# Optimization experiments

Measured on AMD Instinct MI355X. Metric: run time of the kernel, lower is better.

## Reference

```python
import jax, jax.numpy as jnp
import numpy as np

N = 100000
E = 1600000
D_IN = 128
D_OUT = 128
BN_EPS = 1e-5


def setup_inputs() -> dict:
    key = jax.random.key(0)
    k1, k2, k3, k4 = jax.random.split(key, 4)
    x = jax.random.normal(k1, (N, D_IN), dtype=jnp.float32)
    edge_index = jax.random.randint(k2, (2, E), 0, N, dtype=jnp.int64)
    # Linear params (torch: y = x @ W.T + b)
    lim = 1.0 / np.sqrt(D_IN)
    W = jax.random.uniform(k3, (D_OUT, D_IN), minval=-lim, maxval=lim, dtype=jnp.float32)
    b = jax.random.uniform(k4, (D_OUT,), minval=-lim, maxval=lim, dtype=jnp.float32)
    # BatchNorm1d affine params (torch defaults: weight=1, bias=0)
    gamma = jnp.ones((D_OUT,), dtype=jnp.float32)
    beta = jnp.zeros((D_OUT,), dtype=jnp.float32)
    return {"x": x, "edge_index": edge_index, "W": W, "b": b,
            "gamma": gamma, "beta": beta, "batch_size": 32}


def reference(x, edge_index, W, b, gamma, beta, batch_size):
    # Linear
    h = x @ W.T + b  # (N, D_OUT)
    num_nodes = h.shape[0]
    row, col = edge_index[0], edge_index[1]
    # Gather neighbor features and scatter-add into destination rows
    agg = jax.ops.segment_sum(h[col], row, num_segments=num_nodes)  # (N, D_OUT)
    cnt = jax.ops.segment_sum(jnp.ones((edge_index.shape[1], 1), dtype=h.dtype),
                              row, num_segments=num_nodes)  # (N, 1)
    agg = agg / (cnt + 1e-8)
    # Residual
    h = h + agg
    # BatchNorm1d, training mode (batch statistics, biased variance)
    mean = jnp.mean(h, axis=0)
    var = jnp.mean((h - mean) ** 2, axis=0)
    out = (h - mean) * jax.lax.rsqrt(var + BN_EPS) * gamma + beta
    return out
```

## Files before the change

### kernel.cpp

```cpp
#include <hip/hip_runtime.h>

#define BN_EPS_F 1e-5f
#define MAXB 128
#define BIN_CHUNK 4096
#define BIN_EPT 16

typedef __attribute__((ext_vector_type(8))) short bf16x8;
typedef __attribute__((ext_vector_type(4))) float f32x4;

static __device__ __forceinline__ float bf2f(unsigned short u) {
  union { unsigned int i; float f; } c; c.i = ((unsigned int)u) << 16; return c.f;
}
static __device__ __forceinline__ unsigned short f2bf(float f) {
  union { float f; unsigned int i; } c; c.f = f;
  unsigned int r = c.i + 0x7FFFu + ((c.i >> 16) & 1u);
  return (unsigned short)(r >> 16);
}

__global__ void wfrag_kernel(const float* __restrict__ W, unsigned short* __restrict__ wfrag) {
  int idx = blockIdx.x * 256 + threadIdx.x;
  int e = idx & 7, l = (idx >> 3) & 63, kk = (idx >> 9) & 3, jt = idx >> 11;
  int j = jt * 16 + (l & 15);
  int k = kk * 32 + ((l >> 4) << 3) + e;
  wfrag[idx] = f2bf(W[j * 128 + k]);
}

__global__ __launch_bounds__(256) void linear_kernel(
    const float* __restrict__ x, const unsigned short* __restrict__ wfrag,
    const float* __restrict__ bias, ushort4* __restrict__ h4, int n) {
  __shared__ unsigned short els[4][16 * 128];
  const int t = threadIdx.x;
  const int w = t >> 6, lane = t & 63;
  const int base = blockIdx.x * 64 + w * 16;
  const int row = base + (lane & 15);
  const int rowc = row < n ? row : (n - 1);
  const float4* xr = reinterpret_cast<const float4*>(x) + (size_t)rowc * 32;
  const bf16x8* bf = reinterpret_cast<const bf16x8*>(wfrag);

  f32x4 acc[8];
#pragma unroll
  for (int jt = 0; jt < 8; ++jt) acc[jt] = (f32x4){0.f, 0.f, 0.f, 0.f};

#pragma unroll
  for (int kk = 0; kk < 4; ++kk) {
    float4 lo = xr[kk * 8 + ((lane >> 4) << 1)];
    float4 hi = xr[kk * 8 + ((lane >> 4) << 1) + 1];
    bf16x8 a;
    a[0] = (short)f2bf(lo.x); a[1] = (short)f2bf(lo.y);
    a[2] = (short)f2bf(lo.z); a[3] = (short)f2bf(lo.w);
    a[4] = (short)f2bf(hi.x); a[5] = (short)f2bf(hi.y);
    a[6] = (short)f2bf(hi.z); a[7] = (short)f2bf(hi.w);
#pragma unroll
    for (int jt = 0; jt < 8; ++jt) {
      bf16x8 b = bf[(jt * 4 + kk) * 64 + lane];
      acc[jt] = __builtin_amdgcn_mfma_f32_16x16x32_bf16(a, b, acc[jt], 0, 0, 0);
    }
  }

  unsigned short* ep = els[w];
#pragma unroll
  for (int jt = 0; jt < 8; ++jt) {
    float bv = bias[jt * 16 + (lane & 15)];
#pragma unroll
    for (int r = 0; r < 4; ++r) {
      int orow = ((lane >> 4) << 2) + r;
      ep[orow * 128 + jt * 16 + (lane & 15)] = f2bf(acc[jt][r] + bv);
    }
  }
  const ushort4* ep4 = reinterpret_cast<const ushort4*>(ep);
#pragma unroll
  for (int i = 0; i < 8; ++i) {
    int idx = i * 64 + lane;
    int r2 = idx >> 5, c4 = idx & 31;
    int grow = base + r2;
    if (grow < n) h4[(size_t)grow * 32 + c4] = ep4[idx];
  }
}

__global__ __launch_bounds__(256) void bucket_hist_kernel(
    const int* __restrict__ row, int* __restrict__ bhist, int e_total, int nb) {
  __shared__ int bh[MAXB];
  const int t = threadIdx.x;
  if (t < MAXB) bh[t] = 0;
  __syncthreads();
  int i = blockIdx.x * 256 + t;
  const int stride = gridDim.x * 256;
  for (; i < e_total; i += stride) atomicAdd(&bh[row[i] >> 10], 1);
  __syncthreads();
  if (t < nb) {
    int c = bh[t];
    if (c) atomicAdd(&bhist[t], c);
  }
}

__global__ void bucket_scan_kernel(const int* __restrict__ bhist, int* __restrict__ bbase,
                                   int* __restrict__ bcursor, int nb, int e_total) {
  __shared__ int sd[MAXB];
  const int t = threadIdx.x;
  int v = (t < nb) ? bhist[t] : 0;
  sd[t] = v;
  __syncthreads();
  for (int off = 1; off < MAXB; off <<= 1) {
    int u = (t >= off) ? sd[t - off] : 0;
    __syncthreads();
    sd[t] += u;
    __syncthreads();
  }
  int excl = sd[t] - v;
  if (t < nb) { bbase[t] = excl; bcursor[t] = excl; }
  if (t == 0) bbase[nb] = e_total;
}

__global__ __launch_bounds__(256) void bin_kernel(
    const int* __restrict__ row, const int* __restrict__ col,
    int* __restrict__ bcursor, unsigned int* __restrict__ pairs, int e_total, int nb) {
  __shared__ int scount[MAXB];
  __shared__ int gbase[MAXB];
  const int t = threadIdx.x;
  if (t < MAXB) scount[t] = 0;
  __syncthreads();
  const int base = blockIdx.x * BIN_CHUNK;
  int bkt[BIN_EPT], slot[BIN_EPT];
  unsigned int pk[BIN_EPT];
#pragma unroll
  for (int k = 0; k < BIN_EPT; ++k) {
    int i = base + t + (k << 8);
    bkt[k] = -1;
    if (i < e_total) {
      int r = row[i], c = col[i];
      bkt[k] = r >> 10;
      pk[k] = ((unsigned int)(r & 1023) << 17) | (unsigned int)c;
      slot[k] = atomicAdd(&scount[bkt[k]], 1);
    }
  }
  __syncthreads();
  if (t < nb) {
    int c = scount[t];
    gbase[t] = c ? atomicAdd(&bcursor[t], c) : 0;
  }
  __syncthreads();
#pragma unroll
  for (int k = 0; k < BIN_EPT; ++k) {
    if (bkt[k] >= 0) pairs[gbase[bkt[k]] + slot[k]] = pk[k];
  }
}

__global__ __launch_bounds__(256) void csr_kernel(
    const unsigned int* __restrict__ pairs, const int* __restrict__ bbase,
    int* __restrict__ rowptr, int* __restrict__ scol, int n, int e_total) {
  __shared__ int lh[1024];
  __shared__ int sscan[256];
  const int b = blockIdx.x;
  const int t = threadIdx.x;
  const int node_base = b << 10;
  const int nn = min(1024, n - node_base);
  const int p0 = bbase[b], p1 = bbase[b + 1];
  for (int j = t; j < 1024; j += 256) lh[j] = 0;
  __syncthreads();
  for (int i = p0 + t; i < p1; i += 256) {
    atomicAdd(&lh[pairs[i] >> 17], 1);
  }
  __syncthreads();
  const int v0 = lh[4 * t + 0], v1 = lh[4 * t + 1], v2 = lh[4 * t + 2], v3 = lh[4 * t + 3];
  const int s = v0 + v1 + v2 + v3;
  sscan[t] = s;
  __syncthreads();
  for (int off = 1; off < 256; off <<= 1) {
    int u = (t >= off) ? sscan[t - off] : 0;
    __syncthreads();
    sscan[t] += u;
    __syncthreads();
  }
  const int excl = sscan[t] - s;
  const int c0 = excl, c1 = excl + v0, c2 = c1 + v1, c3 = c2 + v2;
  if (4 * t + 0 < nn) rowptr[node_base + 4 * t + 0] = p0 + c0;
  if (4 * t + 1 < nn) rowptr[node_base + 4 * t + 1] = p0 + c1;
  if (4 * t + 2 < nn) rowptr[node_base + 4 * t + 2] = p0 + c2;
  if (4 * t + 3 < nn) rowptr[node_base + 4 * t + 3] = p0 + c3;
  __syncthreads();
  lh[4 * t + 0] = c0; lh[4 * t + 1] = c1; lh[4 * t + 2] = c2; lh[4 * t + 3] = c3;
  __syncthreads();
  for (int i = p0 + t; i < p1; i += 256) {
    unsigned int p = pairs[i];
    int pl = atomicAdd(&lh[p >> 17], 1);
    scol[p0 + pl] = (int)(p & 0x1FFFFu);
  }
  if (b == 0 && t == 0) rowptr[n] = e_total;
}

__global__ __launch_bounds__(256) void agg_kernel(
    const ushort4* __restrict__ h4, const int* __restrict__ rowptr,
    const int* __restrict__ scol, float* __restrict__ out,
    float* __restrict__ stat_sum, float* __restrict__ stat_sumsq, int n_nodes) {
  const int t = threadIdx.x;
  const int wave = t >> 6, lane = t & 63;
  const int half = lane >> 5, q = lane & 31;
  float ls0 = 0.f, ls1 = 0.f, ls2 = 0.f, ls3 = 0.f;
  float lq0 = 0.f, lq1 = 0.f, lq2 = 0.f, lq3 = 0.f;
  const int wstride = gridDim.x << 2;
  for (int node = (blockIdx.x << 2) + wave; node < n_nodes; node += wstride) {
    const int r0 = rowptr[node], r1 = rowptr[node + 1];
    float a0 = 0.f, a1 = 0.f, a2 = 0.f, a3 = 0.f;
    int e = r0 + half;
    for (; e + 2 < r1; e += 4) {
      int c0 = scol[e], c1 = scol[e + 2];
      ushort4 v0 = h4[(size_t)c0 * 32 + q];
      ushort4 v1 = h4[(size_t)c1 * 32 + q];
      a0 += bf2f(v0.x) + bf2f(v1.x);
      a1 += bf2f(v0.y) + bf2f(v1.y);
      a2 += bf2f(v0.z) + bf2f(v1.z);
      a3 += bf2f(v0.w) + bf2f(v1.w);
    }
    if (e < r1) {
      int c0 = scol[e];
      ushort4 v0 = h4[(size_t)c0 * 32 + q];
      a0 += bf2f(v0.x); a1 += bf2f(v0.y); a2 += bf2f(v0.z); a3 += bf2f(v0.w);
    }
    a0 += __shfl_xor(a0, 32, 64);
    a1 += __shfl_xor(a1, 32, 64);
    a2 += __shfl_xor(a2, 32, 64);
    a3 += __shfl_xor(a3, 32, 64);
    if (half == 0) {
      ushort4 hv = h4[(size_t)node * 32 + q];
      const float inv = 1.0f / ((float)(r1 - r0) + 1e-8f);
      float v0 = fmaf(a0, inv, bf2f(hv.x));
      float v1 = fmaf(a1, inv, bf2f(hv.y));
      float v2 = fmaf(a2, inv, bf2f(hv.z));
      float v3 = fmaf(a3, inv, bf2f(hv.w));
      float4 o; o.x = v0; o.y = v1; o.z = v2; o.w = v3;
      *reinterpret_cast<float4*>(&out[(size_t)node * 128 + q * 4]) = o;
      ls0 += v0; ls1 += v1; ls2 += v2; ls3 += v3;
      lq0 = fmaf(v0, v0, lq0); lq1 = fmaf(v1, v1, lq1);
      lq2 = fmaf(v2, v2, lq2); lq3 = fmaf(v3, v3, lq3);
    }
  }
  __shared__ float reds[4][128];
  __shared__ float redq[4][128];
  if (half == 0) {
    float4 s; s.x = ls0; s.y = ls1; s.z = ls2; s.w = ls3;
    float4 qq; qq.x = lq0; qq.y = lq1; qq.z = lq2; qq.w = lq3;
    *reinterpret_cast<float4*>(&reds[wave][q * 4]) = s;
    *reinterpret_cast<float4*>(&redq[wave][q * 4]) = qq;
  }
  __syncthreads();
  if (t < 128) {
    float s = reds[0][t] + reds[1][t] + reds[2][t] + reds[3][t];
    float qv = redq[0][t] + redq[1][t] + redq[2][t] + redq[3][t];
    atomicAdd(&stat_sum[t], s);
    atomicAdd(&stat_sumsq[t], qv);
  }
}

__global__ void finalize_kernel(const float* __restrict__ ssum, const float* __restrict__ ssq,
                                const float* __restrict__ gamma, const float* __restrict__ beta,
                                float* __restrict__ scale, float* __restrict__ shift, int n) {
  const int t = threadIdx.x;
  const float invn = 1.0f / (float)n;
  float mean = ssum[t] * invn;
  float var = ssq[t] * invn - mean * mean;
  float sc = gamma[t] * rsqrtf(var + BN_EPS_F);
  scale[t] = sc;
  shift[t] = beta[t] - mean * sc;
}

__global__ __launch_bounds__(256) void bn_kernel(float* __restrict__ out,
                                                 const float* __restrict__ scale,
                                                 const float* __restrict__ shift, int n_nodes) {
  __shared__ float sc[128], sh[128];
  if (threadIdx.x < 128) {
    sc[threadIdx.x] = scale[threadIdx.x];
    sh[threadIdx.x] = shift[threadIdx.x];
  }
  __syncthreads();
  const int total4 = n_nodes * 32;
  int i = blockIdx.x * 256 + threadIdx.x;
  const int stride = gridDim.x * 256;
  float4* o4 = reinterpret_cast<float4*>(out);
  for (; i < total4; i += stride) {
    float4 v = o4[i];
    const int fq = (i & 31) << 2;
    v.x = fmaf(v.x, sc[fq + 0], sh[fq + 0]);
    v.y = fmaf(v.y, sc[fq + 1], sh[fq + 1]);
    v.z = fmaf(v.z, sc[fq + 2], sh[fq + 2]);
    v.w = fmaf(v.w, sc[fq + 3], sh[fq + 3]);
    o4[i] = v;
  }
}

extern "C" void kernel_launch(void* const* d_in, const int* in_sizes, int n_in,
                              void* d_out, int out_size, void* d_ws, size_t ws_size,
                              hipStream_t stream) {
  const float* x     = (const float*)d_in[0];
  const int*   ei    = (const int*)d_in[1];
  const float* W     = (const float*)d_in[2];
  const float* bias  = (const float*)d_in[3];
  const float* gamma = (const float*)d_in[4];
  const float* beta  = (const float*)d_in[5];
  const int n = in_sizes[0] / 128;
  const int e = in_sizes[1] / 2;
  const int* row = ei;
  const int* col = ei + e;
  float* out = (float*)d_out;

  char* base = (char*)d_ws;
  size_t off = 0;
  auto carve = [&](size_t bytes) -> char* {
    char* p = base + off;
    off += (bytes + 255) & ~(size_t)255;
    return p;
  };
  unsigned short* h = (unsigned short*)carve((size_t)n * 128 * 2);
  unsigned short* wfrag = (unsigned short*)carve(128 * 128 * 2);
  unsigned int* pairs = (unsigned int*)carve((size_t)e * 4);
  int*   scol     = (int*)carve((size_t)e * 4);
  int*   rowptr   = (int*)carve((size_t)(n + 1) * 4);
  int*   bcursor  = (int*)carve(MAXB * 4);
  int*   bbase    = (int*)carve((MAXB + 1) * 4);
  float* scale    = (float*)carve(512);
  float* shift    = (float*)carve(512);
  char*  zbase    = base + off;
  int*   bhist    = (int*)carve(MAXB * 4);
  float* ssum     = (float*)carve(512);
  float* ssq      = (float*)carve(512);
  size_t zlen     = (size_t)((base + off) - zbase);
  (void)ws_size; (void)n_in; (void)out_size;

  const int nb = (n + 1023) >> 10;
  const int bin_grid = (e + BIN_CHUNK - 1) / BIN_CHUNK;
  const int lin_grid = (n + 63) / 64;

  hipMemsetAsync(zbase, 0, zlen, stream);
  wfrag_kernel<<<64, 256, 0, stream>>>(W, wfrag);
  linear_kernel<<<lin_grid, 256, 0, stream>>>(x, wfrag, bias, (ushort4*)h, n);
  bucket_hist_kernel<<<256, 256, 0, stream>>>(row, bhist, e, nb);
  bucket_scan_kernel<<<1, MAXB, 0, stream>>>(bhist, bbase, bcursor, nb, e);
  bin_kernel<<<bin_grid, 256, 0, stream>>>(row, col, bcursor, pairs, e, nb);
  csr_kernel<<<nb, 256, 0, stream>>>(pairs, bbase, rowptr, scol, n, e);
  agg_kernel<<<3200, 256, 0, stream>>>((const ushort4*)h, rowptr, scol, out, ssum, ssq, n);
  finalize_kernel<<<1, 128, 0, stream>>>(ssum, ssq, gamma, beta, scale, shift, n);
  bn_kernel<<<2048, 256, 0, stream>>>(out, scale, shift, n);
}
```

Before: 349.0 us.

## Slice h into feature-major column blocks so aggregation gathers fit in cache

The linear output is stored as 8 slices of 16 features (32 bytes per node per slice). The aggregation kernel assigns each block one slice and one node partition, so the gathered working set per slice (about 3.2 MB) can stay in L2/LLC instead of streaming the full 25 MB table randomly. The intermediate aggregated result is stored in bf16 and converted back in the BN kernel, which halves that round trip but adds a rounding step before normalization. CSR buckets also shrink to 512 nodes, doubling the bucket count, and each gather now moves only 4 bytes per lane, which may raise the instruction overhead per edge.

```diff
diff --git a/kernel.cpp b/kernel.cpp
--- a/kernel.cpp
+++ b/kernel.cpp
@@ -1,9 +1,11 @@
 #include <hip/hip_runtime.h>
 
 #define BN_EPS_F 1e-5f
-#define MAXB 128
+#define MAXB 256
+#define BSHIFT 9
 #define BIN_CHUNK 4096
 #define BIN_EPT 16
+#define NPART 400
 
 typedef __attribute__((ext_vector_type(8))) short bf16x8;
 typedef __attribute__((ext_vector_type(4))) float f32x4;
@@ -27,8 +29,8 @@
 
 __global__ __launch_bounds__(256) void linear_kernel(
     const float* __restrict__ x, const unsigned short* __restrict__ wfrag,
-    const float* __restrict__ bias, ushort4* __restrict__ h4, int n) {
-  __shared__ unsigned short els[4][16 * 128];
+    const float* __restrict__ bias, unsigned short* __restrict__ ht, int n) {
+  __shared__ unsigned short els[4][16 * 132];
   const int t = threadIdx.x;
   const int w = t >> 6, lane = t & 63;
   const int base = blockIdx.x * 64 + w * 16;
@@ -64,16 +66,18 @@
 #pragma unroll
     for (int r = 0; r < 4; ++r) {
       int orow = ((lane >> 4) << 2) + r;
-      ep[orow * 128 + jt * 16 + (lane & 15)] = f2bf(acc[jt][r] + bv);
-    }
-  }
-  const ushort4* ep4 = reinterpret_cast<const ushort4*>(ep);
-#pragma unroll
-  for (int i = 0; i < 8; ++i) {
-    int idx = i * 64 + lane;
-    int r2 = idx >> 5, c4 = idx & 31;
-    int grow = base + r2;
-    if (grow < n) h4[(size_t)grow * 32 + c4] = ep4[idx];
+      ep[orow * 132 + jt * 16 + (lane & 15)] = f2bf(acc[jt][r] + bv);
+    }
+  }
+  const int nl = lane >> 2;
+  const int f4 = (lane & 3) << 2;
+  const int gnode = base + nl;
+#pragma unroll
+  for (int jt = 0; jt < 8; ++jt) {
+    if (gnode < n) {
+      ushort4 v = *reinterpret_cast<const ushort4*>(&ep[nl * 132 + jt * 16 + f4]);
+      *reinterpret_cast<ushort4*>(&ht[((size_t)jt * n + gnode) * 16 + f4]) = v;
+    }
   }
 }
 
@@ -81,11 +85,11 @@
     const int* __restrict__ row, int* __restrict__ bhist, int e_total, int nb) {
   __shared__ int bh[MAXB];
   const int t = threadIdx.x;
-  if (t < MAXB) bh[t] = 0;
+  bh[t] = 0;
   __syncthreads();
   int i = blockIdx.x * 256 + t;
   const int stride = gridDim.x * 256;
-  for (; i < e_total; i += stride) atomicAdd(&bh[row[i] >> 10], 1);
+  for (; i < e_total; i += stride) atomicAdd(&bh[row[i] >> BSHIFT], 1);
   __syncthreads();
   if (t < nb) {
     int c = bh[t];
@@ -117,7 +121,7 @@
   __shared__ int scount[MAXB];
   __shared__ int gbase[MAXB];
   const int t = threadIdx.x;
-  if (t < MAXB) scount[t] = 0;
+  scount[t] = 0;
   __syncthreads();
   const int base = blockIdx.x * BIN_CHUNK;
   int bkt[BIN_EPT], slot[BIN_EPT];
@@ -128,8 +132,8 @@
     bkt[k] = -1;
     if (i < e_total) {
       int r = row[i], c = col[i];
-      bkt[k] = r >> 10;
-      pk[k] = ((unsigned int)(r & 1023) << 17) | (unsigned int)c;
+      bkt[k] = r >> BSHIFT;
+      pk[k] = ((unsigned int)(r & ((1 << BSHIFT) - 1)) << 17) | (unsigned int)c;
       slot[k] = atomicAdd(&scount[bkt[k]], 1);
     }
   }
@@ -148,21 +152,21 @@
 __global__ __launch_bounds__(256) void csr_kernel(
     const unsigned int* __restrict__ pairs, const int* __restrict__ bbase,
     int* __restrict__ rowptr, int* __restrict__ scol, int n, int e_total) {
-  __shared__ int lh[1024];
+  __shared__ int lh[1 << BSHIFT];
   __shared__ int sscan[256];
   const int b = blockIdx.x;
   const int t = threadIdx.x;
-  const int node_base = b << 10;
-  const int nn = min(1024, n - node_base);
+  const int node_base = b << BSHIFT;
+  const int nn = min(1 << BSHIFT, n - node_base);
   const int p0 = bbase[b], p1 = bbase[b + 1];
-  for (int j = t; j < 1024; j += 256) lh[j] = 0;
+  for (int j = t; j < (1 << BSHIFT); j += 256) lh[j] = 0;
   __syncthreads();
   for (int i = p0 + t; i < p1; i += 256) {
     atomicAdd(&lh[pairs[i] >> 17], 1);
   }
   __syncthreads();
-  const int v0 = lh[4 * t + 0], v1 = lh[4 * t + 1], v2 = lh[4 * t + 2], v3 = lh[4 * t + 3];
-  const int s = v0 + v1 + v2 + v3;
+  const int v0 = lh[2 * t + 0], v1 = lh[2 * t + 1];
+  const int s = v0 + v1;
   sscan[t] = s;
   __syncthreads();
   for (int off = 1; off < 256; off <<= 1) {
@@ -172,13 +176,11 @@
     __syncthreads();
   }
   const int excl = sscan[t] - s;
-  const int c0 = excl, c1 = excl + v0, c2 = c1 + v1, c3 = c2 + v2;
-  if (4 * t + 0 < nn) rowptr[node_base + 4 * t + 0] = p0 + c0;
-  if (4 * t + 1 < nn) rowptr[node_base + 4 * t + 1] = p0 + c1;
-  if (4 * t + 2 < nn) rowptr[node_base + 4 * t + 2] = p0 + c2;
-  if (4 * t + 3 < nn) rowptr[node_base + 4 * t + 3] = p0 + c3;
-  __syncthreads();
-  lh[4 * t + 0] = c0; lh[4 * t + 1] = c1; lh[4 * t + 2] = c2; lh[4 * t + 3] = c3;
+  const int c0 = excl, c1 = excl + v0;
+  if (2 * t + 0 < nn) rowptr[node_base + 2 * t + 0] = p0 + c0;
+  if (2 * t + 1 < nn) rowptr[node_base + 2 * t + 1] = p0 + c1;
+  __syncthreads();
+  lh[2 * t + 0] = c0; lh[2 * t + 1] = c1;
   __syncthreads();
   for (int i = p0 + t; i < p1; i += 256) {
     unsigned int p = pairs[i];
@@ -189,65 +191,52 @@
 }
 
 __global__ __launch_bounds__(256) void agg_kernel(
-    const ushort4* __restrict__ h4, const int* __restrict__ rowptr,
-    const int* __restrict__ scol, float* __restrict__ out,
-    float* __restrict__ stat_sum, float* __restrict__ stat_sumsq, int n_nodes) {
+    const ushort2* __restrict__ ht2, const int* __restrict__ rowptr,
+    const int* __restrict__ scol, unsigned short* __restrict__ outp,
+    float* __restrict__ stat_sum, float* __restrict__ stat_sumsq, int n, int npp) {
   const int t = threadIdx.x;
   const int wave = t >> 6, lane = t & 63;
-  const int half = lane >> 5, q = lane & 31;
-  float ls0 = 0.f, ls1 = 0.f, ls2 = 0.f, ls3 = 0.f;
-  float lq0 = 0.f, lq1 = 0.f, lq2 = 0.f, lq3 = 0.f;
-  const int wstride = gridDim.x << 2;
-  for (int node = (blockIdx.x << 2) + wave; node < n_nodes; node += wstride) {
+  const int s = blockIdx.x & 7;
+  const int part = blockIdx.x >> 3;
+  const int f = lane & 7, g = lane >> 3;
+  const size_t sn = (size_t)s * n;
+  const int start = part * npp;
+  const int end = min(n, start + npp);
+  ushort2* op2 = reinterpret_cast<ushort2*>(outp);
+  float ls0 = 0.f, ls1 = 0.f, lq0 = 0.f, lq1 = 0.f;
+  for (int node = start + wave; node < end; node += 4) {
     const int r0 = rowptr[node], r1 = rowptr[node + 1];
-    float a0 = 0.f, a1 = 0.f, a2 = 0.f, a3 = 0.f;
-    int e = r0 + half;
-    for (; e + 2 < r1; e += 4) {
-      int c0 = scol[e], c1 = scol[e + 2];
-      ushort4 v0 = h4[(size_t)c0 * 32 + q];
-      ushort4 v1 = h4[(size_t)c1 * 32 + q];
-      a0 += bf2f(v0.x) + bf2f(v1.x);
-      a1 += bf2f(v0.y) + bf2f(v1.y);
-      a2 += bf2f(v0.z) + bf2f(v1.z);
-      a3 += bf2f(v0.w) + bf2f(v1.w);
-    }
-    if (e < r1) {
-      int c0 = scol[e];
-      ushort4 v0 = h4[(size_t)c0 * 32 + q];
-      a0 += bf2f(v0.x); a1 += bf2f(v0.y); a2 += bf2f(v0.z); a3 += bf2f(v0.w);
-    }
-    a0 += __shfl_xor(a0, 32, 64);
-    a1 += __shfl_xor(a1, 32, 64);
-    a2 += __shfl_xor(a2, 32, 64);
-    a3 += __shfl_xor(a3, 32, 64);
-    if (half == 0) {
-      ushort4 hv = h4[(size_t)node * 32 + q];
+    float a0 = 0.f, a1 = 0.f;
+    for (int e = r0 + g; e < r1; e += 8) {
+      int c = scol[e];
+      ushort2 v = ht2[(sn + c) * 8 + f];
+      a0 += bf2f(v.x); a1 += bf2f(v.y);
+    }
+    a0 += __shfl_xor(a0, 8, 64); a1 += __shfl_xor(a1, 8, 64);
+    a0 += __shfl_xor(a0, 16, 64); a1 += __shfl_xor(a1, 16, 64);
+    a0 += __shfl_xor(a0, 32, 64); a1 += __shfl_xor(a1, 32, 64);
+    if (g == 0) {
+      ushort2 hv = ht2[(sn + node) * 8 + f];
       const float inv = 1.0f / ((float)(r1 - r0) + 1e-8f);
       float v0 = fmaf(a0, inv, bf2f(hv.x));
       float v1 = fmaf(a1, inv, bf2f(hv.y));
-      float v2 = fmaf(a2, inv, bf2f(hv.z));
-      float v3 = fmaf(a3, inv, bf2f(hv.w));
-      float4 o; o.x = v0; o.y = v1; o.z = v2; o.w = v3;
-      *reinterpret_cast<float4*>(&out[(size_t)node * 128 + q * 4]) = o;
-      ls0 += v0; ls1 += v1; ls2 += v2; ls3 += v3;
+      ushort2 o; o.x = f2bf(v0); o.y = f2bf(v1);
+      op2[(sn + node) * 8 + f] = o;
+      ls0 += v0; ls1 += v1;
       lq0 = fmaf(v0, v0, lq0); lq1 = fmaf(v1, v1, lq1);
-      lq2 = fmaf(v2, v2, lq2); lq3 = fmaf(v3, v3, lq3);
-    }
-  }
-  __shared__ float reds[4][128];
-  __shared__ float redq[4][128];
-  if (half == 0) {
-    float4 s; s.x = ls0; s.y = ls1; s.z = ls2; s.w = ls3;
-    float4 qq; qq.x = lq0; qq.y = lq1; qq.z = lq2; qq.w = lq3;
-    *reinterpret_cast<float4*>(&reds[wave][q * 4]) = s;
-    *reinterpret_cast<float4*>(&redq[wave][q * 4]) = qq;
-  }
-  __syncthreads();
-  if (t < 128) {
-    float s = reds[0][t] + reds[1][t] + reds[2][t] + reds[3][t];
-    float qv = redq[0][t] + redq[1][t] + redq[2][t] + redq[3][t];
-    atomicAdd(&stat_sum[t], s);
-    atomicAdd(&stat_sumsq[t], qv);
+    }
+  }
+  __shared__ float rs[4][16], rq[4][16];
+  if (g == 0) {
+    rs[wave][2 * f] = ls0; rs[wave][2 * f + 1] = ls1;
+    rq[wave][2 * f] = lq0; rq[wave][2 * f + 1] = lq1;
+  }
+  __syncthreads();
+  if (t < 16) {
+    float sv = rs[0][t] + rs[1][t] + rs[2][t] + rs[3][t];
+    float qv = rq[0][t] + rq[1][t] + rq[2][t] + rq[3][t];
+    atomicAdd(&stat_sum[s * 16 + t], sv);
+    atomicAdd(&stat_sumsq[s * 16 + t], qv);
   }
 }
 
@@ -263,7 +252,8 @@
   shift[t] = beta[t] - mean * sc;
 }
 
-__global__ __launch_bounds__(256) void bn_kernel(float* __restrict__ out,
+__global__ __launch_bounds__(256) void bn_kernel(const unsigned short* __restrict__ outp,
+                                                 float* __restrict__ out,
                                                  const float* __restrict__ scale,
                                                  const float* __restrict__ shift, int n_nodes) {
   __shared__ float sc[128], sh[128];
@@ -272,18 +262,22 @@
     sh[threadIdx.x] = shift[threadIdx.x];
   }
   __syncthreads();
+  const ushort4* op4 = reinterpret_cast<const ushort4*>(outp);
   const int total4 = n_nodes * 32;
   int i = blockIdx.x * 256 + threadIdx.x;
   const int stride = gridDim.x * 256;
   float4* o4 = reinterpret_cast<float4*>(out);
   for (; i < total4; i += stride) {
-    float4 v = o4[i];
-    const int fq = (i & 31) << 2;
-    v.x = fmaf(v.x, sc[fq + 0], sh[fq + 0]);
-    v.y = fmaf(v.y, sc[fq + 1], sh[fq + 1]);
-    v.z = fmaf(v.z, sc[fq + 2], sh[fq + 2]);
-    v.w = fmaf(v.w, sc[fq + 3], sh[fq + 3]);
-    o4[i] = v;
+    const int node = i >> 5, fq4 = i & 31;
+    const int slice = fq4 >> 2;
+    ushort4 v = op4[((size_t)slice * n_nodes + node) * 4 + (fq4 & 3)];
+    const int fq = fq4 << 2;
+    float4 r;
+    r.x = fmaf(bf2f(v.x), sc[fq + 0], sh[fq + 0]);
+    r.y = fmaf(bf2f(v.y), sc[fq + 1], sh[fq + 1]);
+    r.z = fmaf(bf2f(v.z), sc[fq + 2], sh[fq + 2]);
+    r.w = fmaf(bf2f(v.w), sc[fq + 3], sh[fq + 3]);
+    o4[i] = r;
   }
 }
 
@@ -309,7 +303,8 @@
     off += (bytes + 255) & ~(size_t)255;
     return p;
   };
-  unsigned short* h = (unsigned short*)carve((size_t)n * 128 * 2);
+  unsigned short* ht   = (unsigned short*)carve((size_t)n * 128 * 2);
+  unsigned short* outp = (unsigned short*)carve((size_t)n * 128 * 2);
   unsigned short* wfrag = (unsigned short*)carve(128 * 128 * 2);
   unsigned int* pairs = (unsigned int*)carve((size_t)e * 4);
   int*   scol     = (int*)carve((size_t)e * 4);
@@ -325,18 +320,19 @@
   size_t zlen     = (size_t)((base + off) - zbase);
   (void)ws_size; (void)n_in; (void)out_size;
 
-  const int nb = (n + 1023) >> 10;
+  const int nb = (n + (1 << BSHIFT) - 1) >> BSHIFT;
   const int bin_grid = (e + BIN_CHUNK - 1) / BIN_CHUNK;
   const int lin_grid = (n + 63) / 64;
+  const int npp = (n + NPART - 1) / NPART;
 
   hipMemsetAsync(zbase, 0, zlen, stream);
   wfrag_kernel<<<64, 256, 0, stream>>>(W, wfrag);
-  linear_kernel<<<lin_grid, 256, 0, stream>>>(x, wfrag, bias, (ushort4*)h, n);
+  linear_kernel<<<lin_grid, 256, 0, stream>>>(x, wfrag, bias, ht, n);
   bucket_hist_kernel<<<256, 256, 0, stream>>>(row, bhist, e, nb);
   bucket_scan_kernel<<<1, MAXB, 0, stream>>>(bhist, bbase, bcursor, nb, e);
   bin_kernel<<<bin_grid, 256, 0, stream>>>(row, col, bcursor, pairs, e, nb);
   csr_kernel<<<nb, 256, 0, stream>>>(pairs, bbase, rowptr, scol, n, e);
-  agg_kernel<<<3200, 256, 0, stream>>>((const ushort4*)h, rowptr, scol, out, ssum, ssq, n);
+  agg_kernel<<<8 * NPART, 256, 0, stream>>>((const ushort2*)ht, rowptr, scol, outp, ssum, ssq, n, npp);
   finalize_kernel<<<1, 128, 0, stream>>>(ssum, ssq, gamma, beta, scale, shift, n);
-  bn_kernel<<<2048, 256, 0, stream>>>(out, scale, shift, n);
-}
+  bn_kernel<<<2048, 256, 0, stream>>>(outp, out, scale, shift, n);
+}
```

New measurement: 421.0 us. 20.6% more time.
